# Kernel tuning notes

Measured on AMD Instinct MI355X. Metric: run time of the kernel, lower is better.

The kernel has to match this reference:

```python
import jax, jax.numpy as jnp
import numpy as np

N_E = 1024
E_DIM = 256
BETA = 0.25


def setup_inputs() -> dict:
    key = jax.random.key(0)
    k1, k2 = jax.random.split(key)
    z = jax.random.normal(k1, (32, E_DIM, 2048), dtype=jnp.float32)  # [B, e_dim, T]
    # nn.Embedding weight init: uniform(-1/n_e, 1/n_e)
    embedding = jax.random.uniform(k2, (N_E, E_DIM), dtype=jnp.float32,
                                   minval=-1.0 / N_E, maxval=1.0 / N_E)
    return {"z": z, "embedding": embedding}


def reference(z, embedding):
    # z: [B, e_dim, T] -> [B, T, e_dim]
    zt = jnp.transpose(z, (0, 2, 1))
    B, T, C = zt.shape
    zf = zt.reshape(-1, C)  # [N, e_dim]
    n_e = embedding.shape[0]
    # squared L2 distances via ||a||^2 + ||b||^2 - 2 a.b  -> [N, n_e]
    d = (jnp.sum(zf * zf, axis=1, keepdims=True)
         + jnp.sum(embedding * embedding, axis=1)
         - 2.0 * jnp.matmul(zf, embedding.T))
    idx = jnp.argmin(d, axis=1)  # [N]
    # one-hot @ embedding == direct gather
    z_q = embedding[idx].reshape(B, T, C)
    loss = (BETA * jnp.mean((jax.lax.stop_gradient(z_q) - zt) ** 2)
            + jnp.mean((z_q - jax.lax.stop_gradient(zt)) ** 2))
    # straight-through estimator
    z_q_st = zt + jax.lax.stop_gradient(z_q - zt)
    # e_mean = mean of one-hot encodings == normalized code usage counts
    counts = jnp.zeros((n_e,), dtype=zf.dtype).at[idx].add(1.0)
    e_mean = counts / idx.shape[0]
    perplexity = jnp.exp(-jnp.sum(e_mean * jnp.log(e_mean + 1e-10)))
    z_q_out = jnp.transpose(z_q_st, (0, 2, 1))  # back to [B, e_dim, T]
    return (z_q_out, loss, perplexity, idx)
```

## Files before the change

kernel.cpp:

```cpp
#include <hip/hip_runtime.h>

#define B_ 32
#define C_ 256
#define T_ 2048
#define N_ 65536
#define NE_ 1024
#define NELEM 16777216
#define TAU 1.75e-4f
#define WLCAP 8192
#define RPB 8

typedef _Float16 half8 __attribute__((ext_vector_type(8)));
typedef float f32x4 __attribute__((ext_vector_type(4)));


__global__ void k_prep(const float* __restrict__ emb, half8* __restrict__ ebuf,
                       float* __restrict__ enorm, float* __restrict__ et) {
  int code = blockIdx.x * blockDim.x + threadIdx.x;
  const float4* row = reinterpret_cast<const float4*>(emb + (size_t)code * C_);
  double sum = 0.0;
#pragma unroll
  for (int k = 0; k < C_ / 4; ++k) {
    float4 v = row[k];
    sum = fma((double)v.x, (double)v.x, sum);
    sum = fma((double)v.y, (double)v.y, sum);
    sum = fma((double)v.z, (double)v.z, sum);
    sum = fma((double)v.w, (double)v.w, sum);
    et[(k * 4 + 0) * NE_ + code] = v.x;
    et[(k * 4 + 1) * NE_ + code] = v.y;
    et[(k * 4 + 2) * NE_ + code] = v.z;
    et[(k * 4 + 3) * NE_ + code] = v.w;
  }
  enorm[code] = (float)sum;
  const int ct = code >> 4, c = code & 15;
#pragma unroll
  for (int s = 0; s < 8; ++s) {
#pragma unroll
    for (int g = 0; g < 4; ++g) {
      float4 v0 = row[s * 8 + g * 2];
      float4 v1 = row[s * 8 + g * 2 + 1];
      half8 hv;
      hv[0] = (_Float16)v0.x; hv[1] = (_Float16)v0.y;
      hv[2] = (_Float16)v0.z; hv[3] = (_Float16)v0.w;
      hv[4] = (_Float16)v1.x; hv[5] = (_Float16)v1.y;
      hv[6] = (_Float16)v1.z; hv[7] = (_Float16)v1.w;
      ebuf[(ct * 8 + s) * 64 + g * 16 + c] = hv;
    }
  }
}

__launch_bounds__(256, 2)
__global__ void k_vq(const float* __restrict__ z, const half8* __restrict__ ebuf,
                     const float* __restrict__ enorm, int* __restrict__ idx_i,
                     float* __restrict__ idx_f, int* __restrict__ counts,
                     int* __restrict__ nflag, int* __restrict__ worklist) {
  const int tid = threadIdx.x;
  const int w = tid >> 6;
  const int l = tid & 63;
  const int col = l & 15;
  const int g = l >> 4;
  const int n0 = blockIdx.x * 128;
  const int b = n0 >> 11;
  const int t0 = (n0 & (T_ - 1)) + w * 32;
  const float* zc0 = z + (size_t)b * C_ * T_ + t0 + col;
  const float* zc1 = zc0 + 16;

  half8 A0[8], A1[8];
#pragma unroll
  for (int s = 0; s < 8; ++s) {
    half8 h0, h1;
#pragma unroll
    for (int i = 0; i < 8; ++i) {
      const size_t ko = (size_t)(32 * s + 8 * g + i) * T_;
      h0[i] = (_Float16)zc0[ko];
      h1[i] = (_Float16)zc1[ko];
    }
    A0[s] = h0; A1[s] = h1;
  }

  float b1s[2][4], b2s[2][4]; int b1i[2][4];
#pragma unroll
  for (int rt = 0; rt < 2; ++rt)
#pragma unroll
    for (int q = 0; q < 4; ++q) { b1s[rt][q] = 3.4e38f; b2s[rt][q] = 3.4e38f; b1i[rt][q] = 0; }

  auto fold = [&](const f32x4& c00, const f32x4& c10, const f32x4& c01, const f32x4& c11,
                  float en0, float en1, int cb0, int cb1) {
#pragma unroll
    for (int q = 0; q < 4; ++q) {
      {
        float sc = fmaf(-2.f, c00[q], en0);
        float nb2 = fminf(b2s[0][q], fmaxf(b1s[0][q], sc));
        bool lt = sc < b1s[0][q];
        b2s[0][q] = nb2; b1i[0][q] = lt ? cb0 : b1i[0][q]; b1s[0][q] = fminf(b1s[0][q], sc);
      }
      {
        float sc = fmaf(-2.f, c10[q], en0);
        float nb2 = fminf(b2s[1][q], fmaxf(b1s[1][q], sc));
        bool lt = sc < b1s[1][q];
        b2s[1][q] = nb2; b1i[1][q] = lt ? cb0 : b1i[1][q]; b1s[1][q] = fminf(b1s[1][q], sc);
      }
      {
        float sc = fmaf(-2.f, c01[q], en1);
        float nb2 = fminf(b2s[0][q], fmaxf(b1s[0][q], sc));
        bool lt = sc < b1s[0][q];
        b2s[0][q] = nb2; b1i[0][q] = lt ? cb1 : b1i[0][q]; b1s[0][q] = fminf(b1s[0][q], sc);
      }
      {
        float sc = fmaf(-2.f, c11[q], en1);
        float nb2 = fminf(b2s[1][q], fmaxf(b1s[1][q], sc));
        bool lt = sc < b1s[1][q];
        b2s[1][q] = nb2; b1i[1][q] = lt ? cb1 : b1i[1][q]; b1s[1][q] = fminf(b1s[1][q], sc);
      }
    }
  };

  const half8* bp = ebuf + l;
  half8 Bf0[8], Bf1[8];
#pragma unroll
  for (int s = 0; s < 8; ++s) { Bf0[s] = bp[s * 64]; Bf1[s] = bp[(8 + s) * 64]; }
  const f32x4 zero4 = {0.f, 0.f, 0.f, 0.f};

  for (int ctp = 0; ctp < 32; ++ctp) {
    f32x4 a00 = zero4, a01 = zero4, a10 = zero4, a11 = zero4;
#pragma unroll
    for (int s = 0; s < 8; ++s) {
      a00 = __builtin_amdgcn_mfma_f32_16x16x32_f16(A0[s], Bf0[s], a00, 0, 0, 0);
      a10 = __builtin_amdgcn_mfma_f32_16x16x32_f16(A1[s], Bf0[s], a10, 0, 0, 0);
    }
    if (ctp < 31) {
#pragma unroll
      for (int s = 0; s < 8; ++s) Bf0[s] = bp[((ctp + 1) * 16 + s) * 64];
    }
#pragma unroll
    for (int s = 0; s < 8; ++s) {
      a01 = __builtin_amdgcn_mfma_f32_16x16x32_f16(A0[s], Bf1[s], a01, 0, 0, 0);
      a11 = __builtin_amdgcn_mfma_f32_16x16x32_f16(A1[s], Bf1[s], a11, 0, 0, 0);
    }
    if (ctp < 31) {
#pragma unroll
      for (int s = 0; s < 8; ++s) Bf1[s] = bp[((ctp + 1) * 16 + 8 + s) * 64];
    }
    const float en0 = enorm[ctp * 32 + col];
    const float en1 = enorm[ctp * 32 + 16 + col];
    fold(a00, a10, a01, a11, en0, en1, ctp * 32 + col, ctp * 32 + 16 + col);
  }

#pragma unroll
  for (int m = 1; m < 16; m <<= 1) {
#pragma unroll
    for (int rt = 0; rt < 2; ++rt)
#pragma unroll
      for (int q = 0; q < 4; ++q) {
        float o1 = __shfl_xor(b1s[rt][q], m);
        int oi = __shfl_xor(b1i[rt][q], m);
        float o2 = __shfl_xor(b2s[rt][q], m);
        float hi = fmaxf(b1s[rt][q], o1);
        b2s[rt][q] = fminf(fminf(b2s[rt][q], o2), hi);
        if (o1 < b1s[rt][q] || (o1 == b1s[rt][q] && oi < b1i[rt][q])) {
          b1s[rt][q] = o1; b1i[rt][q] = oi;
        }
      }
  }
  if (col == 0) {
#pragma unroll
    for (int rt = 0; rt < 2; ++rt)
#pragma unroll
      for (int q = 0; q < 4; ++q) {
        int n = n0 + w * 32 + rt * 16 + g * 4 + q;
        idx_i[n] = b1i[rt][q];
        idx_f[n] = (float)b1i[rt][q];
        atomicAdd(&counts[b1i[rt][q]], 1);
        if (b2s[rt][q] - b1s[rt][q] < TAU) {
          int p = atomicAdd(nflag, 1);
          if (p < WLCAP) worklist[p] = n;
        }
      }
  }
}

__global__ void k_zstage(const float* __restrict__ z, const int* __restrict__ nflag,
                         const int* __restrict__ worklist, float* __restrict__ zstage,
                         float* __restrict__ szfbuf) {
  __shared__ double wred[4];
  const int tid = threadIdx.x;
  int cnt = nflag[0];
  if (cnt > WLCAP) cnt = WLCAP;
  for (int wi = blockIdx.x; wi < cnt; wi += gridDim.x) {
    int n = worklist[wi];
    int b = n >> 11, t = n & (T_ - 1);
    float zv = z[(size_t)b * C_ * T_ + (size_t)tid * T_ + t];
    zstage[(size_t)wi * C_ + tid] = zv;
    double p = (double)zv * (double)zv;
#pragma unroll
    for (int m = 32; m > 0; m >>= 1) p += __shfl_down(p, m);
    if ((tid & 63) == 0) wred[tid >> 6] = p;
    __syncthreads();
    if (tid == 0)
      szfbuf[wi] = (float)(wred[0] + wred[1] + wred[2] + wred[3]);
    __syncthreads();
  }
}

__global__ void k_repair(const float* __restrict__ zstage, const float* __restrict__ szfbuf,
                         const float* __restrict__ et, const float* __restrict__ enorm,
                         const int* __restrict__ nflag, const int* __restrict__ worklist,
                         unsigned long long* __restrict__ keys) {
  __shared__ float zs[RPB][C_];
  __shared__ unsigned long long kred[RPB][256];
  const int tid = threadIdx.x;
  int cnt = nflag[0];
  if (cnt > WLCAP) cnt = WLCAP;
  const int ngroups = (cnt + RPB - 1) / RPB;
  const int nunits = ngroups * 4;
  for (int u = blockIdx.x; u < nunits; u += gridDim.x) {
    const int grp = u >> 2;
    const int quarter = u & 3;
    const int base = grp * RPB;
#pragma unroll
    for (int r = 0; r < RPB; ++r) {
      int wi = base + r; if (wi >= cnt) wi = cnt - 1;
      zs[r][tid] = zstage[(size_t)wi * C_ + tid];
    }
    __syncthreads();
    const int j = quarter * 256 + tid;
    float acc[RPB];
#pragma unroll
    for (int r = 0; r < RPB; ++r) acc[r] = 0.f;
#pragma unroll 4
    for (int k4 = 0; k4 < C_ / 4; ++k4) {
      float e0 = et[(k4 * 4 + 0) * NE_ + j];
      float e1 = et[(k4 * 4 + 1) * NE_ + j];
      float e2 = et[(k4 * 4 + 2) * NE_ + j];
      float e3 = et[(k4 * 4 + 3) * NE_ + j];
#pragma unroll
      for (int r = 0; r < RPB; ++r) {
        acc[r] = fmaf(zs[r][k4 * 4 + 0], e0, acc[r]);
        acc[r] = fmaf(zs[r][k4 * 4 + 1], e1, acc[r]);
        acc[r] = fmaf(zs[r][k4 * 4 + 2], e2, acc[r]);
        acc[r] = fmaf(zs[r][k4 * 4 + 3], e3, acc[r]);
      }
    }
    const float en = enorm[j];
#pragma unroll
    for (int r = 0; r < RPB; ++r) {
      int wi = base + r; if (wi >= cnt) wi = cnt - 1;
      float X = szfbuf[wi] + en;
      float Y = 2.0f * acc[r];
      float d = X - Y;
      unsigned int du = __float_as_uint(d);
      unsigned int sortable = (du & 0x80000000u) ? ~du : (du | 0x80000000u);
      kred[r][tid] = ((unsigned long long)sortable << 32) | (unsigned int)j;
    }
    __syncthreads();
    for (int o = 128; o > 0; o >>= 1) {
      if (tid < o) {
#pragma unroll
        for (int r = 0; r < RPB; ++r) {
          unsigned long long ok = kred[r][tid + o];
          if (ok < kred[r][tid]) kred[r][tid] = ok;
        }
      }
      __syncthreads();
    }
    if (tid < RPB && base + tid < cnt)
      atomicMin(&keys[base + tid], kred[tid][0]);
    __syncthreads();
  }
}

__global__ void k_fix(const int* __restrict__ nflag, const int* __restrict__ worklist,
                      const unsigned long long* __restrict__ keys,
                      int* __restrict__ idx_i, float* __restrict__ idx_f,
                      int* __restrict__ counts) {
  int cnt = nflag[0];
  if (cnt > WLCAP) cnt = WLCAP;
  int wi = blockIdx.x * blockDim.x + threadIdx.x;
  if (wi < cnt) {
    int n = worklist[wi];
    int nw = (int)(keys[wi] & 0xFFFFFFFFull);
    int old = idx_i[n];
    if (nw != old) {
      idx_i[n] = nw; idx_f[n] = (float)nw;
      atomicAdd(&counts[old], -1);
      atomicAdd(&counts[nw], 1);
    }
  }
}

__launch_bounds__(256, 4)
__global__ void k_gather(const float* __restrict__ z, const float* __restrict__ emb,
                         const int* __restrict__ idxv, float* __restrict__ zq,
                         float* __restrict__ sse) {
  __shared__ int ids[32];
  __shared__ float tile[32 * 260];
  __shared__ float wsum[4];
  const int tid = threadIdx.x;
  const int blk = blockIdx.x;
  const int b = blk >> 6;
  const int t0 = (blk & 63) << 5;
  const int n0 = (b << 11) + t0;
  if (tid < 32) ids[tid] = idxv[n0 + tid];
  __syncthreads();
  const int r = tid & 31;
  const int q = tid >> 5;
  {
    const float4* er = reinterpret_cast<const float4*>(emb) + ((size_t)ids[r] << 6) + (q << 3);
    float4* dst = reinterpret_cast<float4*>(&tile[r * 260 + (q << 5)]);
#pragma unroll
    for (int j = 0; j < 8; ++j) dst[j] = er[j];
  }
  __syncthreads();
  float local = 0.f;
  const size_t base = (((size_t)b << 8) << 11) + t0;
#pragma unroll 8
  for (int it = 0; it < 32; ++it) {
    const int c = (it << 3) + q;
    const float qv = tile[r * 260 + c];
    const size_t gofs = base + ((size_t)c << 11) + r;
    const float zv = z[gofs];
    zq[gofs] = qv;
    const float d = qv - zv;
    local = fmaf(d, d, local);
  }
#pragma unroll
  for (int m = 32; m > 0; m >>= 1) local += __shfl_down(local, m);
  if ((tid & 63) == 0) wsum[tid >> 6] = local;
  __syncthreads();
  if (tid == 0) atomicAdd(sse, wsum[0] + wsum[1] + wsum[2] + wsum[3]);
}

__global__ void k_final(const int* __restrict__ counts, const float* __restrict__ sse,
                        float* __restrict__ out_loss, float* __restrict__ out_perp) {
  __shared__ float red[256];
  int tid = threadIdx.x;
  float s = 0.f;
  for (int j = tid; j < NE_; j += 256) {
    float em = (float)counts[j] * (1.0f / (float)N_);
    s += em * logf(em + 1e-10f);
  }
  red[tid] = s;
  __syncthreads();
  for (int o = 128; o > 0; o >>= 1) {
    if (tid < o) red[tid] += red[tid + o];
    __syncthreads();
  }
  if (tid == 0) {
    out_perp[0] = expf(-red[0]);
    out_loss[0] = (0.25f + 1.0f) * sse[0] / (float)NELEM;
  }
}

extern "C" void kernel_launch(void* const* d_in, const int* in_sizes, int n_in,
                              void* d_out, int out_size, void* d_ws, size_t ws_size,
                              hipStream_t stream) {
  const float* z = (const float*)d_in[0];
  const float* emb = (const float*)d_in[1];
  float* out = (float*)d_out;
  float* zq_out = out;
  float* out_loss = out + NELEM;
  float* out_perp = out + NELEM + 1;
  float* out_idx = out + NELEM + 2;

  int* ws_counts = (int*)d_ws;
  float* ws_enorm = (float*)d_ws + 1024;
  float* ws_sse = (float*)d_ws + 2048;
  int* ws_nflag = (int*)d_ws + 2049;
  unsigned long long* ws_keys = (unsigned long long*)((float*)d_ws + 2056);
  int* ws_idx = (int*)d_ws + 18440;
  int* ws_worklist = (int*)d_ws + 83976;
  float* ws_szf = (float*)d_ws + 92168;
  half8* ws_ebuf = (half8*)((float*)d_ws + 100360);
  float* ws_et = (float*)d_ws + 231432;
  float* ws_zstage = (float*)d_ws + 493576;

  hipMemsetAsync(d_ws, 0, 8224, stream);
  hipMemsetAsync((char*)d_ws + 8224, 0xFF, WLCAP * 8, stream);

  k_prep<<<NE_ / 256, 256, 0, stream>>>(emb, ws_ebuf, ws_enorm, ws_et);
  k_vq<<<N_ / 128, 256, 0, stream>>>(z, ws_ebuf, ws_enorm, ws_idx, out_idx,
                                     ws_counts, ws_nflag, ws_worklist);
  k_zstage<<<2048, 256, 0, stream>>>(z, ws_nflag, ws_worklist, ws_zstage, ws_szf);
  k_repair<<<2048, 256, 0, stream>>>(ws_zstage, ws_szf, ws_et, ws_enorm,
                                     ws_nflag, ws_worklist, ws_keys);
  k_fix<<<WLCAP / 256, 256, 0, stream>>>(ws_nflag, ws_worklist, ws_keys,
                                         ws_idx, out_idx, ws_counts);
  k_gather<<<2048, 256, 0, stream>>>(z, emb, ws_idx, zq_out, ws_sse);
  k_final<<<1, 256, 0, stream>>>(ws_counts, ws_sse, out_loss, out_perp);
}
```

Before: 205.2 us.

## Double rows per wave in VQ kernel to reuse codebook fragments

Each wave in the nearest-code kernel now holds four 16-row tiles of z instead of two, so each loaded codebook fragment feeds four MFMAs rather than two. This halves the codebook traffic per row and halves the grid size. The cost is more registers: launch bounds drop to one block per CU, and with 256 blocks there is less occupancy to hide the latency of loading z.

```diff
diff --git a/kernel.cpp b/kernel.cpp
--- a/kernel.cpp
+++ b/kernel.cpp
@@ -49,7 +49,7 @@
   }
 }
 
-__launch_bounds__(256, 2)
+__launch_bounds__(256, 1)
 __global__ void k_vq(const float* __restrict__ z, const half8* __restrict__ ebuf,
                      const float* __restrict__ enorm, int* __restrict__ idx_i,
                      float* __restrict__ idx_f, int* __restrict__ counts,
@@ -59,61 +59,30 @@
   const int l = tid & 63;
   const int col = l & 15;
   const int g = l >> 4;
-  const int n0 = blockIdx.x * 128;
+  const int n0 = blockIdx.x * 256;
   const int b = n0 >> 11;
-  const int t0 = (n0 & (T_ - 1)) + w * 32;
-  const float* zc0 = z + (size_t)b * C_ * T_ + t0 + col;
-  const float* zc1 = zc0 + 16;
-
-  half8 A0[8], A1[8];
-#pragma unroll
-  for (int s = 0; s < 8; ++s) {
-    half8 h0, h1;
-#pragma unroll
-    for (int i = 0; i < 8; ++i) {
-      const size_t ko = (size_t)(32 * s + 8 * g + i) * T_;
-      h0[i] = (_Float16)zc0[ko];
-      h1[i] = (_Float16)zc1[ko];
-    }
-    A0[s] = h0; A1[s] = h1;
-  }
-
-  float b1s[2][4], b2s[2][4]; int b1i[2][4];
-#pragma unroll
-  for (int rt = 0; rt < 2; ++rt)
+  const int t0 = (n0 & (T_ - 1)) + w * 64;
+  const float* zbase = z + (size_t)b * C_ * T_ + t0 + col;
+
+  half8 A[4][8];
+#pragma unroll
+  for (int rt = 0; rt < 4; ++rt) {
+    const float* zc = zbase + rt * 16;
+#pragma unroll
+    for (int s = 0; s < 8; ++s) {
+      half8 hv;
+#pragma unroll
+      for (int i = 0; i < 8; ++i)
+        hv[i] = (_Float16)zc[(size_t)(32 * s + 8 * g + i) * T_];
+      A[rt][s] = hv;
+    }
+  }
+
+  float b1s[4][4], b2s[4][4]; int b1i[4][4];
+#pragma unroll
+  for (int rt = 0; rt < 4; ++rt)
 #pragma unroll
     for (int q = 0; q < 4; ++q) { b1s[rt][q] = 3.4e38f; b2s[rt][q] = 3.4e38f; b1i[rt][q] = 0; }
-
-  auto fold = [&](const f32x4& c00, const f32x4& c10, const f32x4& c01, const f32x4& c11,
-                  float en0, float en1, int cb0, int cb1) {
-#pragma unroll
-    for (int q = 0; q < 4; ++q) {
-      {
-        float sc = fmaf(-2.f, c00[q], en0);
-        float nb2 = fminf(b2s[0][q], fmaxf(b1s[0][q], sc));
-        bool lt = sc < b1s[0][q];
-        b2s[0][q] = nb2; b1i[0][q] = lt ? cb0 : b1i[0][q]; b1s[0][q] = fminf(b1s[0][q], sc);
-      }
-      {
-        float sc = fmaf(-2.f, c10[q], en0);
-        float nb2 = fminf(b2s[1][q], fmaxf(b1s[1][q], sc));
-        bool lt = sc < b1s[1][q];
-        b2s[1][q] = nb2; b1i[1][q] = lt ? cb0 : b1i[1][q]; b1s[1][q] = fminf(b1s[1][q], sc);
-      }
-      {
-        float sc = fmaf(-2.f, c01[q], en1);
-        float nb2 = fminf(b2s[0][q], fmaxf(b1s[0][q], sc));
-        bool lt = sc < b1s[0][q];
-        b2s[0][q] = nb2; b1i[0][q] = lt ? cb1 : b1i[0][q]; b1s[0][q] = fminf(b1s[0][q], sc);
-      }
-      {
-        float sc = fmaf(-2.f, c11[q], en1);
-        float nb2 = fminf(b2s[1][q], fmaxf(b1s[1][q], sc));
-        bool lt = sc < b1s[1][q];
-        b2s[1][q] = nb2; b1i[1][q] = lt ? cb1 : b1i[1][q]; b1s[1][q] = fminf(b1s[1][q], sc);
-      }
-    }
-  };
 
   const half8* bp = ebuf + l;
   half8 Bf0[8], Bf1[8];
@@ -122,11 +91,15 @@
   const f32x4 zero4 = {0.f, 0.f, 0.f, 0.f};
 
   for (int ctp = 0; ctp < 32; ++ctp) {
-    f32x4 a00 = zero4, a01 = zero4, a10 = zero4, a11 = zero4;
+    f32x4 a0[4], a1[4];
+#pragma unroll
+    for (int rt = 0; rt < 4; ++rt) { a0[rt] = zero4; a1[rt] = zero4; }
 #pragma unroll
     for (int s = 0; s < 8; ++s) {
-      a00 = __builtin_amdgcn_mfma_f32_16x16x32_f16(A0[s], Bf0[s], a00, 0, 0, 0);
-      a10 = __builtin_amdgcn_mfma_f32_16x16x32_f16(A1[s], Bf0[s], a10, 0, 0, 0);
+      a0[0] = __builtin_amdgcn_mfma_f32_16x16x32_f16(A[0][s], Bf0[s], a0[0], 0, 0, 0);
+      a0[1] = __builtin_amdgcn_mfma_f32_16x16x32_f16(A[1][s], Bf0[s], a0[1], 0, 0, 0);
+      a0[2] = __builtin_amdgcn_mfma_f32_16x16x32_f16(A[2][s], Bf0[s], a0[2], 0, 0, 0);
+      a0[3] = __builtin_amdgcn_mfma_f32_16x16x32_f16(A[3][s], Bf0[s], a0[3], 0, 0, 0);
     }
     if (ctp < 31) {
 #pragma unroll
@@ -134,8 +107,10 @@
     }
 #pragma unroll
     for (int s = 0; s < 8; ++s) {
-      a01 = __builtin_amdgcn_mfma_f32_16x16x32_f16(A0[s], Bf1[s], a01, 0, 0, 0);
-      a11 = __builtin_amdgcn_mfma_f32_16x16x32_f16(A1[s], Bf1[s], a11, 0, 0, 0);
+      a1[0] = __builtin_amdgcn_mfma_f32_16x16x32_f16(A[0][s], Bf1[s], a1[0], 0, 0, 0);
+      a1[1] = __builtin_amdgcn_mfma_f32_16x16x32_f16(A[1][s], Bf1[s], a1[1], 0, 0, 0);
+      a1[2] = __builtin_amdgcn_mfma_f32_16x16x32_f16(A[2][s], Bf1[s], a1[2], 0, 0, 0);
+      a1[3] = __builtin_amdgcn_mfma_f32_16x16x32_f16(A[3][s], Bf1[s], a1[3], 0, 0, 0);
     }
     if (ctp < 31) {
 #pragma unroll
@@ -143,13 +118,30 @@
     }
     const float en0 = enorm[ctp * 32 + col];
     const float en1 = enorm[ctp * 32 + 16 + col];
-    fold(a00, a10, a01, a11, en0, en1, ctp * 32 + col, ctp * 32 + 16 + col);
+    const int cb0 = ctp * 32 + col, cb1 = ctp * 32 + 16 + col;
+#pragma unroll
+    for (int q = 0; q < 4; ++q) {
+#pragma unroll
+      for (int rt = 0; rt < 4; ++rt) {
+        float sc = fmaf(-2.f, a0[rt][q], en0);
+        float nb2 = fminf(b2s[rt][q], fmaxf(b1s[rt][q], sc));
+        bool lt = sc < b1s[rt][q];
+        b2s[rt][q] = nb2; b1i[rt][q] = lt ? cb0 : b1i[rt][q]; b1s[rt][q] = fminf(b1s[rt][q], sc);
+      }
+#pragma unroll
+      for (int rt = 0; rt < 4; ++rt) {
+        float sc = fmaf(-2.f, a1[rt][q], en1);
+        float nb2 = fminf(b2s[rt][q], fmaxf(b1s[rt][q], sc));
+        bool lt = sc < b1s[rt][q];
+        b2s[rt][q] = nb2; b1i[rt][q] = lt ? cb1 : b1i[rt][q]; b1s[rt][q] = fminf(b1s[rt][q], sc);
+      }
+    }
   }
 
 #pragma unroll
   for (int m = 1; m < 16; m <<= 1) {
 #pragma unroll
-    for (int rt = 0; rt < 2; ++rt)
+    for (int rt = 0; rt < 4; ++rt)
 #pragma unroll
       for (int q = 0; q < 4; ++q) {
         float o1 = __shfl_xor(b1s[rt][q], m);
@@ -164,10 +156,10 @@
   }
   if (col == 0) {
 #pragma unroll
-    for (int rt = 0; rt < 2; ++rt)
+    for (int rt = 0; rt < 4; ++rt)
 #pragma unroll
       for (int q = 0; q < 4; ++q) {
-        int n = n0 + w * 32 + rt * 16 + g * 4 + q;
+        int n = n0 + w * 64 + rt * 16 + g * 4 + q;
         idx_i[n] = b1i[rt][q];
         idx_f[n] = (float)b1i[rt][q];
         atomicAdd(&counts[b1i[rt][q]], 1);
@@ -378,7 +370,7 @@
   hipMemsetAsync((char*)d_ws + 8224, 0xFF, WLCAP * 8, stream);
 
   k_prep<<<NE_ / 256, 256, 0, stream>>>(emb, ws_ebuf, ws_enorm, ws_et);
-  k_vq<<<N_ / 128, 256, 0, stream>>>(z, ws_ebuf, ws_enorm, ws_idx, out_idx,
+  k_vq<<<N_ / 256, 256, 0, stream>>>(z, ws_ebuf, ws_enorm, ws_idx, out_idx,
                                      ws_counts, ws_nflag, ws_worklist);
   k_zstage<<<2048, 256, 0, stream>>>(z, ws_nflag, ws_worklist, ws_zstage, ws_szf);
   k_repair<<<2048, 256, 0, stream>>>(ws_zstage, ws_szf, ws_et, ws_enorm,
```

Result: slower. 229.8 us (+12.0%).

## Fold loss SSE into VQ distance kernel and stage codebook tiles via LDS

Applied to the files above, without the earlier changes.

The loss sum of squared errors is now derived from the argmin distance plus the row norm of z computed in k_vq, with flagged rows using the exact repaired key distance in k_fix. This lets k_gather skip re-reading z entirely, halving its memory traffic. The codebook tiles in k_vq are now double-buffered through shared memory with global_load_lds instead of per-wave register loads, which cuts redundant global reads across waves but adds a barrier per tile. k_prep also launches with smaller blocks. The loss now relies on fp16-MFMA distances for non-flagged rows, which risks small numerical differences.

```diff
diff --git a/kernel.cpp b/kernel.cpp
--- a/kernel.cpp
+++ b/kernel.cpp
@@ -49,11 +49,25 @@
   }
 }
 
+__device__ __forceinline__ void stage_tile(const half8* __restrict__ ebuf,
+                                           half8* bsbase, int ctp, int w, int l) {
+#pragma unroll
+  for (int j = 0; j < 4; ++j) {
+    const half8* gp = ebuf + (size_t)ctp * 1024 + (w * 4 + j) * 64 + l;
+    half8* lp = bsbase + (w * 4 + j) * 64;
+    __builtin_amdgcn_global_load_lds(
+        (const __attribute__((address_space(1))) unsigned int*)gp,
+        (__attribute__((address_space(3))) unsigned int*)lp, 16, 0, 0);
+  }
+}
+
 __launch_bounds__(256, 2)
 __global__ void k_vq(const float* __restrict__ z, const half8* __restrict__ ebuf,
                      const float* __restrict__ enorm, int* __restrict__ idx_i,
                      float* __restrict__ idx_f, int* __restrict__ counts,
-                     int* __restrict__ nflag, int* __restrict__ worklist) {
+                     int* __restrict__ nflag, int* __restrict__ worklist,
+                     float* __restrict__ sse) {
+  __shared__ half8 Bs[2][1024];
   const int tid = threadIdx.x;
   const int w = tid >> 6;
   const int l = tid & 63;
@@ -65,18 +79,26 @@
   const float* zc0 = z + (size_t)b * C_ * T_ + t0 + col;
   const float* zc1 = zc0 + 16;
 
+  stage_tile(ebuf, &Bs[0][0], 0, w, l);
+
   half8 A0[8], A1[8];
+  float s0 = 0.f, s1 = 0.f;
 #pragma unroll
   for (int s = 0; s < 8; ++s) {
     half8 h0, h1;
 #pragma unroll
     for (int i = 0; i < 8; ++i) {
       const size_t ko = (size_t)(32 * s + 8 * g + i) * T_;
-      h0[i] = (_Float16)zc0[ko];
-      h1[i] = (_Float16)zc1[ko];
+      float zf0 = zc0[ko], zf1 = zc1[ko];
+      h0[i] = (_Float16)zf0;
+      h1[i] = (_Float16)zf1;
+      s0 = fmaf(zf0, zf0, s0);
+      s1 = fmaf(zf1, zf1, s1);
     }
     A0[s] = h0; A1[s] = h1;
   }
+  s0 += __shfl_xor(s0, 16); s0 += __shfl_xor(s0, 32);
+  s1 += __shfl_xor(s1, 16); s1 += __shfl_xor(s1, 32);
 
   float b1s[2][4], b2s[2][4]; int b1i[2][4];
 #pragma unroll
@@ -84,66 +106,58 @@
 #pragma unroll
     for (int q = 0; q < 4; ++q) { b1s[rt][q] = 3.4e38f; b2s[rt][q] = 3.4e38f; b1i[rt][q] = 0; }
 
-  auto fold = [&](const f32x4& c00, const f32x4& c10, const f32x4& c01, const f32x4& c11,
-                  float en0, float en1, int cb0, int cb1) {
+  const f32x4 zero4 = {0.f, 0.f, 0.f, 0.f};
+  __syncthreads();
+
+  int cur = 0;
+  for (int ctp = 0; ctp < 32; ++ctp) {
+    if (ctp < 31) stage_tile(ebuf, &Bs[cur ^ 1][0], ctp + 1, w, l);
+    const half8* bp = &Bs[cur][l];
+    f32x4 a00 = zero4, a01 = zero4, a10 = zero4, a11 = zero4;
+#pragma unroll
+    for (int s = 0; s < 8; ++s) {
+      half8 bf = bp[s * 64];
+      a00 = __builtin_amdgcn_mfma_f32_16x16x32_f16(A0[s], bf, a00, 0, 0, 0);
+      a10 = __builtin_amdgcn_mfma_f32_16x16x32_f16(A1[s], bf, a10, 0, 0, 0);
+    }
+#pragma unroll
+    for (int s = 0; s < 8; ++s) {
+      half8 bf = bp[(8 + s) * 64];
+      a01 = __builtin_amdgcn_mfma_f32_16x16x32_f16(A0[s], bf, a01, 0, 0, 0);
+      a11 = __builtin_amdgcn_mfma_f32_16x16x32_f16(A1[s], bf, a11, 0, 0, 0);
+    }
+    const float en0 = enorm[ctp * 32 + col];
+    const float en1 = enorm[ctp * 32 + 16 + col];
+    const int cb0 = ctp * 32 + col, cb1 = ctp * 32 + 16 + col;
 #pragma unroll
     for (int q = 0; q < 4; ++q) {
       {
-        float sc = fmaf(-2.f, c00[q], en0);
+        float sc = fmaf(-2.f, a00[q], en0);
         float nb2 = fminf(b2s[0][q], fmaxf(b1s[0][q], sc));
         bool lt = sc < b1s[0][q];
         b2s[0][q] = nb2; b1i[0][q] = lt ? cb0 : b1i[0][q]; b1s[0][q] = fminf(b1s[0][q], sc);
       }
       {
-        float sc = fmaf(-2.f, c10[q], en0);
+        float sc = fmaf(-2.f, a10[q], en0);
         float nb2 = fminf(b2s[1][q], fmaxf(b1s[1][q], sc));
         bool lt = sc < b1s[1][q];
         b2s[1][q] = nb2; b1i[1][q] = lt ? cb0 : b1i[1][q]; b1s[1][q] = fminf(b1s[1][q], sc);
       }
       {
-        float sc = fmaf(-2.f, c01[q], en1);
+        float sc = fmaf(-2.f, a01[q], en1);
         float nb2 = fminf(b2s[0][q], fmaxf(b1s[0][q], sc));
         bool lt = sc < b1s[0][q];
         b2s[0][q] = nb2; b1i[0][q] = lt ? cb1 : b1i[0][q]; b1s[0][q] = fminf(b1s[0][q], sc);
       }
       {
-        float sc = fmaf(-2.f, c11[q], en1);
+        float sc = fmaf(-2.f, a11[q], en1);
         float nb2 = fminf(b2s[1][q], fmaxf(b1s[1][q], sc));
         bool lt = sc < b1s[1][q];
         b2s[1][q] = nb2; b1i[1][q] = lt ? cb1 : b1i[1][q]; b1s[1][q] = fminf(b1s[1][q], sc);
       }
     }
-  };
-
-  const half8* bp = ebuf + l;
-  half8 Bf0[8], Bf1[8];
-#pragma unroll
-  for (int s = 0; s < 8; ++s) { Bf0[s] = bp[s * 64]; Bf1[s] = bp[(8 + s) * 64]; }
-  const f32x4 zero4 = {0.f, 0.f, 0.f, 0.f};
-
-  for (int ctp = 0; ctp < 32; ++ctp) {
-    f32x4 a00 = zero4, a01 = zero4, a10 = zero4, a11 = zero4;
-#pragma unroll
-    for (int s = 0; s < 8; ++s) {
-      a00 = __builtin_amdgcn_mfma_f32_16x16x32_f16(A0[s], Bf0[s], a00, 0, 0, 0);
-      a10 = __builtin_amdgcn_mfma_f32_16x16x32_f16(A1[s], Bf0[s], a10, 0, 0, 0);
-    }
-    if (ctp < 31) {
-#pragma unroll
-      for (int s = 0; s < 8; ++s) Bf0[s] = bp[((ctp + 1) * 16 + s) * 64];
-    }
-#pragma unroll
-    for (int s = 0; s < 8; ++s) {
-      a01 = __builtin_amdgcn_mfma_f32_16x16x32_f16(A0[s], Bf1[s], a01, 0, 0, 0);
-      a11 = __builtin_amdgcn_mfma_f32_16x16x32_f16(A1[s], Bf1[s], a11, 0, 0, 0);
-    }
-    if (ctp < 31) {
-#pragma unroll
-      for (int s = 0; s < 8; ++s) Bf1[s] = bp[((ctp + 1) * 16 + 8 + s) * 64];
-    }
-    const float en0 = enorm[ctp * 32 + col];
-    const float en1 = enorm[ctp * 32 + 16 + col];
-    fold(a00, a10, a01, a11, en0, en1, ctp * 32 + col, ctp * 32 + 16 + col);
+    __syncthreads();
+    cur ^= 1;
   }
 
 #pragma unroll
@@ -162,7 +176,14 @@
         }
       }
   }
+  float rsum[2][4];
+#pragma unroll
+  for (int q = 0; q < 4; ++q) {
+    rsum[0][q] = __shfl(s0, g * 4 + q);
+    rsum[1][q] = __shfl(s1, g * 4 + q);
+  }
   if (col == 0) {
+    float local = 0.f;
 #pragma unroll
     for (int rt = 0; rt < 2; ++rt)
 #pragma unroll
@@ -174,8 +195,11 @@
         if (b2s[rt][q] - b1s[rt][q] < TAU) {
           int p = atomicAdd(nflag, 1);
           if (p < WLCAP) worklist[p] = n;
+        } else {
+          local += rsum[rt][q] + b1s[rt][q];
         }
       }
+    atomicAdd(sse, local);
   }
 }
 
@@ -272,13 +296,17 @@
 __global__ void k_fix(const int* __restrict__ nflag, const int* __restrict__ worklist,
                       const unsigned long long* __restrict__ keys,
                       int* __restrict__ idx_i, float* __restrict__ idx_f,
-                      int* __restrict__ counts) {
+                      int* __restrict__ counts, float* __restrict__ sse) {
   int cnt = nflag[0];
   if (cnt > WLCAP) cnt = WLCAP;
   int wi = blockIdx.x * blockDim.x + threadIdx.x;
   if (wi < cnt) {
     int n = worklist[wi];
-    int nw = (int)(keys[wi] & 0xFFFFFFFFull);
+    unsigned long long key = keys[wi];
+    int nw = (int)(key & 0xFFFFFFFFull);
+    unsigned int s = (unsigned int)(key >> 32);
+    unsigned int du = (s & 0x80000000u) ? (s & 0x7FFFFFFFu) : ~s;
+    atomicAdd(sse, __uint_as_float(du));
     int old = idx_i[n];
     if (nw != old) {
       idx_i[n] = nw; idx_f[n] = (float)nw;
@@ -289,12 +317,10 @@
 }
 
 __launch_bounds__(256, 4)
-__global__ void k_gather(const float* __restrict__ z, const float* __restrict__ emb,
-                         const int* __restrict__ idxv, float* __restrict__ zq,
-                         float* __restrict__ sse) {
+__global__ void k_gather(const float* __restrict__ emb, const int* __restrict__ idxv,
+                         float* __restrict__ zq) {
   __shared__ int ids[32];
   __shared__ float tile[32 * 260];
-  __shared__ float wsum[4];
   const int tid = threadIdx.x;
   const int blk = blockIdx.x;
   const int b = blk >> 6;
@@ -311,23 +337,12 @@
     for (int j = 0; j < 8; ++j) dst[j] = er[j];
   }
   __syncthreads();
-  float local = 0.f;
   const size_t base = (((size_t)b << 8) << 11) + t0;
 #pragma unroll 8
   for (int it = 0; it < 32; ++it) {
     const int c = (it << 3) + q;
-    const float qv = tile[r * 260 + c];
-    const size_t gofs = base + ((size_t)c << 11) + r;
-    const float zv = z[gofs];
-    zq[gofs] = qv;
-    const float d = qv - zv;
-    local = fmaf(d, d, local);
-  }
-#pragma unroll
-  for (int m = 32; m > 0; m >>= 1) local += __shfl_down(local, m);
-  if ((tid & 63) == 0) wsum[tid >> 6] = local;
-  __syncthreads();
-  if (tid == 0) atomicAdd(sse, wsum[0] + wsum[1] + wsum[2] + wsum[3]);
+    zq[base + ((size_t)c << 11) + r] = tile[r * 260 + c];
+  }
 }
 
 __global__ void k_final(const int* __restrict__ counts, const float* __restrict__ sse,
@@ -377,14 +392,14 @@
   hipMemsetAsync(d_ws, 0, 8224, stream);
   hipMemsetAsync((char*)d_ws + 8224, 0xFF, WLCAP * 8, stream);
 
-  k_prep<<<NE_ / 256, 256, 0, stream>>>(emb, ws_ebuf, ws_enorm, ws_et);
+  k_prep<<<NE_ / 64, 64, 0, stream>>>(emb, ws_ebuf, ws_enorm, ws_et);
   k_vq<<<N_ / 128, 256, 0, stream>>>(z, ws_ebuf, ws_enorm, ws_idx, out_idx,
-                                     ws_counts, ws_nflag, ws_worklist);
+                                     ws_counts, ws_nflag, ws_worklist, ws_sse);
   k_zstage<<<2048, 256, 0, stream>>>(z, ws_nflag, ws_worklist, ws_zstage, ws_szf);
   k_repair<<<2048, 256, 0, stream>>>(ws_zstage, ws_szf, ws_et, ws_enorm,
                                      ws_nflag, ws_worklist, ws_keys);
   k_fix<<<WLCAP / 256, 256, 0, stream>>>(ws_nflag, ws_worklist, ws_keys,
-                                         ws_idx, out_idx, ws_counts);
-  k_gather<<<2048, 256, 0, stream>>>(z, emb, ws_idx, zq_out, ws_sse);
+                                         ws_idx, out_idx, ws_counts, ws_sse);
+  k_gather<<<2048, 256, 0, stream>>>(emb, ws_idx, zq_out);
   k_final<<<1, 256, 0, stream>>>(ws_counts, ws_sse, out_loss, out_perp);
 }
```

Result: faster. 185.4 us (-9.6%).
